# Performance work log

Measured on AMD Instinct MI355X. Metric: run time of the kernel, lower is better.

## Reference

```python
import jax, jax.numpy as jnp
import numpy as np

IMG = 224
BLK = 8
POOL = 7


def dct_matrix(n=BLK):
    # Orthonormal DCT-II matrix: dct(v, norm='ortho') == D @ v
    k = jnp.arange(n, dtype=jnp.float32)[:, None]
    m = jnp.arange(n, dtype=jnp.float32)[None, :]
    D = jnp.cos(jnp.pi * (2.0 * m + 1.0) * k / (2.0 * n)) * jnp.sqrt(2.0 / n)
    return D.at[0].mul(1.0 / jnp.sqrt(2.0))


def conv3x3(x, w, b):
    # NCHW, OIHW, stride 1, SAME padding
    y = jax.lax.conv_general_dilated(x, w, (1, 1), 'SAME',
                                     dimension_numbers=('NCHW', 'OIHW', 'NCHW'))
    return y + b[None, :, None, None]


def adaptive_pool7(x):
    # [B,C,224,224] -> [B,C,7,7] via mean over 32x32 windows
    B, C, H, W = x.shape
    return x.reshape(B, C, POOL, H // POOL, POOL, W // POOL).mean(axis=(3, 5))


def setup_inputs() -> dict:
    key = jax.random.key(0)
    ks = jax.random.split(key, 7)
    B = 32
    x = jax.random.uniform(ks[0], (B, 3, IMG, IMG), dtype=jnp.float32)
    s = 0.02
    return {
        'x': x,
        'dct_w': jax.random.normal(ks[1], (64, 3, 3, 3), jnp.float32) * s,
        'dct_b': jnp.zeros((64,), jnp.float32),
        'fft_w': jax.random.normal(ks[2], (64, 6, 3, 3), jnp.float32) * s,
        'fft_b': jnp.zeros((64,), jnp.float32),
        'fc_w': jax.random.normal(ks[3], (512, 2 * 64 * POOL * POOL), jnp.float32) * s,
        'fc_b': jnp.zeros((512,), jnp.float32),
    }


def reference(x, dct_w, dct_b, fft_w, fft_b, fc_w, fc_b):
    B = x.shape[0]
    # ---- DCT branch ----
    # grayscale (RGB2GRAY) scaled to 0..255 (uint8 cast omitted for differentiability)
    gray = (0.299 * x[:, 0] + 0.587 * x[:, 1] + 0.114 * x[:, 2]) * 255.0  # [B,H,W]
    nb = (IMG - BLK) // BLK  # 27: loop range(0, H-8, 8) skips the last block row/col
    g = gray[:, :nb * BLK, :nb * BLK].reshape(B, nb, BLK, nb, BLK)
    blocks = g.transpose(0, 1, 3, 2, 4).reshape(B, nb * nb, BLK, BLK)
    D = dct_matrix()
    dct_blocks = jnp.einsum('ij,bnjk,lk->bnil', D, blocks, D)  # 2D ortho DCT per block
    dct_img = dct_blocks.mean(axis=1)  # [B,8,8]
    dct_resized = jax.image.resize(dct_img, (B, IMG, IMG), method='linear')
    dct_in = jnp.broadcast_to(dct_resized[:, None], (B, 3, IMG, IMG))
    dct_pooled = adaptive_pool7(conv3x3(dct_in, dct_w, dct_b)).reshape(B, -1)

    # ---- FFT branch ----
    f = jnp.fft.fft2(x)  # [B,3,H,W] complex
    # channel order: real0, imag0, real1, imag1, real2, imag2
    fft_in = jnp.stack([f.real.astype(jnp.float32), f.imag.astype(jnp.float32)],
                       axis=2).reshape(B, 6, IMG, IMG)
    fft_pooled = adaptive_pool7(conv3x3(fft_in, fft_w, fft_b)).reshape(B, -1)

    combined = jnp.concatenate([dct_pooled, fft_pooled], axis=1)  # [B,6272]
    return jax.nn.relu(combined @ fc_w.T + fc_b)
```

## Files before the change

kernel.cpp:

```cpp
#include <hip/hip_runtime.h>
#include <math.h>

#define IMG 224
#define NR  21

__device__ __forceinline__ void range_lohi(int r, int& lo, int& hi) {
    int py = r / 3, s = (r % 3) - 1;
    lo = 32 * py + s; hi = lo + 32;
    if (lo < 0) lo = 0;
    if (hi > IMG) hi = IMG;
}

__device__ __forceinline__ float2 geom_range(int lo, int len, int y,
                                             const float* c0, const float* s0) {
    if (y == 0) return make_float2((float)len, 0.f);
    int i0 = (lo * y) % IMG;
    int iL = (len * y) % IMG;
    float w0x = c0[i0], w0y = s0[i0];
    float wLx = c0[iL], wLy = s0[iL];
    float w1x = c0[y],  w1y = s0[y];
    float nx = w0x * (1.f - wLx) + w0y * wLy;
    float ny = w0y * (1.f - wLx) - w0x * wLy;
    float dx = 1.f - w1x, dy = -w1y;
    float inv = 1.f / (dx * dx + dy * dy);
    return make_float2((nx * dx + ny * dy) * inv, (ny * dx - nx * dy) * inv);
}

__device__ __forceinline__ void build_cis(float* c0, float* s0, int t) {
    if (t < IMG) {
        double ang = 2.0 * M_PI * (double)t / (double)IMG;
        c0[t] = (float)cos(ang);
        s0[t] = (float)(-sin(ang));
    }
}

__global__ __launch_bounds__(256) void ka_rowdft_gray(const float* __restrict__ x,
        const float* __restrict__ dct_w,
        float2* __restrict__ T, float* __restrict__ meansum,
        float* __restrict__ afold_g, float* __restrict__ Dm_g,
        float* __restrict__ wsum3_g)
{
    __shared__ __align__(16) char smem[39424];
    int t = threadIdx.x;
    int blk = blockIdx.x;

    if (blk < 336) {
        float2* sA = (float2*)smem;
        float*  c0 = (float*)(smem + 37632);
        float*  s0 = c0 + IMG;
        build_cis(c0, s0, t);
        __syncthreads();
        for (int i = t; i < NR * IMG; i += 256) {
            int r = i / IMG, y = i % IMG;
            int lo, hi; range_lohi(r, lo, hi);
            sA[i] = geom_range(lo, hi - lo, y, c0, s0);
        }
        __syncthreads();

        int part = t >> 6;
        int lane = t & 63;
        int row = blk * 64 + lane;
        const float* src = x + (size_t)row * IMG + part * 56;

        float2 acc[NR];
        #pragma unroll
        for (int c = 0; c < NR; ++c) acc[c] = make_float2(0.f, 0.f);

        for (int i = 0; i < 56; i += 4) {
            float4 v = *(const float4*)(src + i);
            #pragma unroll
            for (int c = 0; c < NR; ++c) {
                const float2* ap = &sA[c * IMG + part * 56 + i];
                float2 a0 = ap[0], a1 = ap[1], a2 = ap[2], a3 = ap[3];
                acc[c].x += v.x * a0.x + v.y * a1.x + v.z * a2.x + v.w * a3.x;
                acc[c].y += v.x * a0.y + v.y * a1.y + v.z * a2.y + v.w * a3.y;
            }
        }

        __syncthreads();
        float2* red = (float2*)smem;
        if (part > 0) {
            float2* dst = red + ((size_t)(part - 1) * 64 + lane) * NR;
            #pragma unroll
            for (int c = 0; c < NR; ++c) dst[c] = acc[c];
        }
        __syncthreads();
        if (part == 0) {
            #pragma unroll
            for (int c = 0; c < NR; ++c) {
                float2 s = acc[c];
                float2 p1 = red[((size_t)0 * 64 + lane) * NR + c];
                float2 p2 = red[((size_t)1 * 64 + lane) * NR + c];
                float2 p3 = red[((size_t)2 * 64 + lane) * NR + c];
                s.x += p1.x + p2.x + p3.x;
                s.y += p1.y + p2.y + p3.y;
                T[(size_t)row * NR + c] = s;
            }
        }
    } else if (blk < 592) {
        int bb = blk - 336;
        int b = bb >> 3, j = bb & 7;
        float* sm = (float*)smem;
        if (t < 216) {
            const float* pr = x + (size_t)(b * 3 + 0) * IMG * IMG;
            const float* pg = x + (size_t)(b * 3 + 1) * IMG * IMG;
            const float* pb = x + (size_t)(b * 3 + 2) * IMG * IMG;
            float acc = 0.f;
            for (int by = 0; by < 27; ++by) {
                int o = (8 * by + j) * IMG + t;
                acc += 76.245f * pr[o] + 149.685f * pg[o] + 29.07f * pb[o];
            }
            sm[t] = acc;
        }
        __syncthreads();
        if (t < 8) {
            float s = 0.f;
            for (int q = t; q < 216; q += 8) s += sm[q];
            meansum[(b * 8 + j) * 8 + t] = s;
        }
    } else {
        if (t < NR * 8) {
            int r = t / 8, j = t % 8;
            int lo, hi; range_lohi(r, lo, hi);
            double s = 0.0;
            for (int y = lo; y < hi; ++y) {
                double sf = (y + 0.5) / 28.0 - 0.5;
                double w = 1.0 - fabs(sf - (double)j);
                if (w < 0.0) w = 0.0;
                double tot = 0.0;
                for (int jj = 0; jj < 8; ++jj) {
                    double wj = 1.0 - fabs(sf - (double)jj);
                    if (wj > 0.0) tot += wj;
                }
                s += w / tot;
            }
            afold_g[t] = (float)s;
        }
        if (t >= 192 && t < 256) {
            int i = t - 192, k = i / 8, m = i % 8;
            double v = cos(M_PI * (2.0 * m + 1.0) * k / 16.0) * 0.5;
            if (k == 0) v *= 0.70710678118654752440;
            Dm_g[i] = (float)v;
        }
        for (int i = t; i < 64 * 9; i += 256) {
            int cout = i / 9, q = i % 9;
            float s = 0.f;
            for (int cin = 0; cin < 3; ++cin) s += dct_w[(cout * 3 + cin) * 9 + q];
            wsum3_g[i] = s;
        }
    }
}

__global__ __launch_bounds__(256) void kb_fold(const float2* __restrict__ T,
        float2* __restrict__ rs2)
{
    __shared__ __align__(16) char smem[39424];
    float*  c0  = (float*)smem;
    float*  s0  = c0 + IMG;
    float2* sAh = (float2*)(smem + 1792);
    float2* sT  = (float2*)(smem + 20608);

    int blk = blockIdx.x, t = threadIdx.x;
    int b = blk / 6, rem = blk % 6;
    int cin = rem >> 1, half = rem & 1;

    build_cis(c0, s0, t);
    __syncthreads();
    for (int i = t; i < NR * 112; i += 256) {
        int rr = i / 112, y = half * 112 + (i % 112);
        int lo, hi; range_lohi(rr, lo, hi);
        sAh[i] = geom_range(lo, hi - lo, y, c0, s0);
    }
    const float2* Tbase = T + ((size_t)(b * 3 + cin) * IMG + half * 112) * NR;
    for (int i = t; i < 112 * NR; i += 256) sT[i] = Tbase[i];
    __syncthreads();

    float2* dst = rs2 + (size_t)((b * 3 + cin) * 2 + half) * NR * NR;
    for (int p = t; p < NR * NR; p += 256) {
        int rr = p / NR, cc = p % NR;
        float re = 0.f, im = 0.f;
        const float2* arow = &sAh[rr * 112];
        for (int y = 0; y < 112; ++y) {
            float2 a  = arow[y];
            float2 tv = sT[y * NR + cc];
            re += a.x * tv.x - a.y * tv.y;
            im += a.x * tv.y + a.y * tv.x;
        }
        dst[p] = make_float2(re, im);
    }
}

__global__ __launch_bounds__(256) void kb_asm(const float2* __restrict__ rs2,
        const float* __restrict__ meansum, const float* __restrict__ afold_g,
        const float* __restrict__ Dm_g, const float* __restrict__ wsum3_g,
        const float* __restrict__ dct_b, const float* __restrict__ fft_w,
        const float* __restrict__ fft_b, float* __restrict__ PT)
{
    __shared__ __align__(16) char smem[24576];
    int blk = blockIdx.x, t = threadIdx.x;
    int b = blk >> 1, which = blk & 1;
    const float inv = 1.0f / 1024.0f;

    if (which == 0) {
        float* WSd  = (float*)smem;
        float* Msc  = WSd + 441;
        float* dimg = Msc + 64;
        float* Ds   = dimg + 64;
        float* af   = Ds + 64;
        float* sws  = af + 168;
        if (t < 64) { Ds[t] = Dm_g[t]; Msc[t] = meansum[b * 64 + t] * (1.0f / 729.0f); }
        if (t < NR * 8) af[t] = afold_g[t];
        for (int i = t; i < 64 * 9; i += 256) sws[i] = wsum3_g[i];
        __syncthreads();
        if (t < 64) {
            int i = t / 8, l = t % 8;
            float s = 0.f;
            for (int j = 0; j < 8; ++j) {
                float rj = 0.f;
                for (int k = 0; k < 8; ++k) rj += Msc[j * 8 + k] * Ds[l * 8 + k];
                s += Ds[i * 8 + j] * rj;
            }
            dimg[t] = s;
        }
        __syncthreads();
        for (int p = t; p < NR * NR; p += 256) {
            int rr = p / NR, cc = p % NR;
            float s = 0.f;
            for (int j = 0; j < 8; ++j) {
                float rj = 0.f;
                for (int k = 0; k < 8; ++k) rj += dimg[j * 8 + k] * af[cc * 8 + k];
                s += af[rr * 8 + j] * rj;
            }
            WSd[p] = s;
        }
        __syncthreads();
        for (int i = t; i < 3136; i += 256) {
            int cout = i / 49, q = i % 49, py = q / 7, px = q % 7;
            float s = 0.f;
            #pragma unroll
            for (int ky = 0; ky < 3; ++ky)
                #pragma unroll
                for (int kx = 0; kx < 3; ++kx)
                    s += sws[cout * 9 + ky * 3 + kx] * WSd[(py * 3 + ky) * NR + (px * 3 + kx)];
            PT[(size_t)i * 32 + b] = dct_b[cout] + s * inv;
        }
    } else {
        float2* RSs = (float2*)smem;
        float*  sfw = (float*)(smem + 10584);
        for (int i = t; i < 3 * NR * NR; i += 256) {
            int cin = i / (NR * NR), p = i % (NR * NR);
            float2 v0 = rs2[(size_t)((b * 3 + cin) * 2 + 0) * NR * NR + p];
            float2 v1 = rs2[(size_t)((b * 3 + cin) * 2 + 1) * NR * NR + p];
            RSs[i] = make_float2(v0.x + v1.x, v0.y + v1.y);
        }
        for (int i = t; i < 64 * 6 * 9; i += 256) sfw[i] = fft_w[i];
        __syncthreads();
        for (int i = t; i < 3136; i += 256) {
            int cout = i / 49, q = i % 49, py = q / 7, px = q % 7;
            float s = 0.f;
            for (int cin = 0; cin < 3; ++cin) {
                #pragma unroll
                for (int ky = 0; ky < 3; ++ky)
                    #pragma unroll
                    for (int kx = 0; kx < 3; ++kx) {
                        float2 v = RSs[cin * NR * NR + (py * 3 + ky) * NR + (px * 3 + kx)];
                        const float* wp = &sfw[(cout * 6 + 2 * cin) * 9 + ky * 3 + kx];
                        s += wp[0] * v.x + wp[9] * v.y;
                    }
            }
            PT[(size_t)(3136 + i) * 32 + b] = fft_b[cout] + s * inv;
        }
    }
}

__global__ __launch_bounds__(256) void kc_fc(const float* __restrict__ PT,
        const float* __restrict__ fc_w, float* __restrict__ part)
{
    int oc = blockIdx.x / 14;
    int kc = blockIdx.x % 14;
    int t = threadIdx.x;
    int b = t & 31, sub = t >> 5;
    int o0 = oc * 4;
    int k0 = kc * 448 + sub * 56;

    const float* w0 = fc_w + (size_t)(o0 + 0) * 6272 + k0;
    const float* w1 = fc_w + (size_t)(o0 + 1) * 6272 + k0;
    const float* w2 = fc_w + (size_t)(o0 + 2) * 6272 + k0;
    const float* w3 = fc_w + (size_t)(o0 + 3) * 6272 + k0;
    const float* p  = PT + (size_t)k0 * 32 + b;

    float a0 = 0.f, a1 = 0.f, a2 = 0.f, a3 = 0.f;
    #pragma unroll 2
    for (int k = 0; k < 56; k += 4) {
        float4 v0 = *(const float4*)(w0 + k);
        float4 v1 = *(const float4*)(w1 + k);
        float4 v2 = *(const float4*)(w2 + k);
        float4 v3 = *(const float4*)(w3 + k);
        float p0 = p[(k + 0) * 32];
        float p1 = p[(k + 1) * 32];
        float p2 = p[(k + 2) * 32];
        float p3 = p[(k + 3) * 32];
        a0 += p0 * v0.x + p1 * v0.y + p2 * v0.z + p3 * v0.w;
        a1 += p0 * v1.x + p1 * v1.y + p2 * v1.z + p3 * v1.w;
        a2 += p0 * v2.x + p1 * v2.y + p2 * v2.z + p3 * v2.w;
        a3 += p0 * v3.x + p1 * v3.y + p2 * v3.z + p3 * v3.w;
    }

    __shared__ float sm[8 * 128];
    sm[sub * 128 +  0 + b] = a0;
    sm[sub * 128 + 32 + b] = a1;
    sm[sub * 128 + 64 + b] = a2;
    sm[sub * 128 + 96 + b] = a3;
    __syncthreads();
    if (t < 128) {
        int oi = t >> 5, b2 = t & 31;
        float s = 0.f;
        #pragma unroll
        for (int c = 0; c < 8; ++c) s += sm[c * 128 + oi * 32 + b2];
        part[(size_t)kc * 16384 + (size_t)(o0 + oi) * 32 + b2] = s;
    }
}

__global__ __launch_bounds__(256) void kc_out(const float* __restrict__ part,
        const float* __restrict__ fc_b, float* __restrict__ out)
{
    int idx = blockIdx.x * 256 + threadIdx.x;
    int o = idx >> 5, b = idx & 31;
    float s = fc_b[o];
    #pragma unroll
    for (int c = 0; c < 14; ++c) s += part[(size_t)c * 16384 + idx];
    out[(size_t)b * 512 + o] = fmaxf(s, 0.f);
}

extern "C" void kernel_launch(void* const* d_in, const int* in_sizes, int n_in,
                              void* d_out, int out_size, void* d_ws, size_t ws_size,
                              hipStream_t stream)
{
    const float* x     = (const float*)d_in[0];
    const float* dct_w = (const float*)d_in[1];
    const float* dct_b = (const float*)d_in[2];
    const float* fft_w = (const float*)d_in[3];
    const float* fft_b = (const float*)d_in[4];
    const float* fc_w  = (const float*)d_in[5];
    const float* fc_b  = (const float*)d_in[6];
    float* out = (float*)d_out;

    char* ws = (char*)d_ws;
    size_t off = 0;
    auto alloc = [&](size_t bytes) {
        char* p = ws + off;
        off = (off + bytes + 255) & ~(size_t)255;
        return p;
    };
    float2* T       = (float2*)alloc((size_t)21504 * NR * 8);
    float*  meansum = (float*) alloc(32 * 64 * 4);
    float*  afold_g = (float*) alloc(NR * 8 * 4);
    float*  Dm_g    = (float*) alloc(64 * 4);
    float*  wsum3_g = (float*) alloc(64 * 9 * 4);
    float2* rs2     = (float2*)alloc((size_t)192 * NR * NR * 8);
    float*  PT      = (float*) alloc((size_t)6272 * 32 * 4);
    float*  part    = (float*) alloc((size_t)14 * 512 * 32 * 4);
    (void)ws_size; (void)in_sizes; (void)n_in; (void)out_size;

    hipLaunchKernelGGL(ka_rowdft_gray, dim3(593),  dim3(256), 0, stream,
                       x, dct_w, T, meansum, afold_g, Dm_g, wsum3_g);
    hipLaunchKernelGGL(kb_fold,        dim3(192),  dim3(256), 0, stream, T, rs2);
    hipLaunchKernelGGL(kb_asm,         dim3(64),   dim3(256), 0, stream,
                       rs2, meansum, afold_g, Dm_g, wsum3_g, dct_b, fft_w, fft_b, PT);
    hipLaunchKernelGGL(kc_fc,          dim3(1792), dim3(256), 0, stream, PT, fc_w, part);
    hipLaunchKernelGGL(kc_out,         dim3(64),   dim3(256), 0, stream, part, fc_b, out);
}
```

Baseline: 147.0 us.

## Exploit real-input DFT symmetry and precompute twiddle-range table in separate kernel

Moves construction of the summed-twiddle coefficient table out of every row-DFT block into a tiny pre-kernel that writes real and imaginary tables to global memory. The row DFT now folds each real input row into symmetric (x[n]+x[N-n]) and antisymmetric parts, so only half the coefficients (113 of 224) are needed per output and the multiply count is roughly halved. This removes the per-block redundant table build and two barriers, and reads coefficients from global/cache instead of shared memory. It adds an extra kernel launch and relies on the range-summed coefficients having the conjugate symmetry that the split assumes.

```diff
diff --git a/kernel.cpp b/kernel.cpp
--- a/kernel.cpp
+++ b/kernel.cpp
@@ -34,50 +34,76 @@
     }
 }
 
+__global__ __launch_bounds__(256) void k0_tab(float* __restrict__ are,
+                                              float* __restrict__ aim)
+{
+    __shared__ float c0[IMG], s0[IMG];
+    int t = threadIdx.x;
+    build_cis(c0, s0, t);
+    __syncthreads();
+    int r = blockIdx.x;
+    int lo, hi; range_lohi(r, lo, hi);
+    if (t < 116) {
+        float2 a = (t < 113) ? geom_range(lo, hi - lo, t, c0, s0)
+                             : make_float2(0.f, 0.f);
+        are[r * 116 + t] = a.x;
+        aim[r * 116 + t] = a.y;
+    }
+}
+
 __global__ __launch_bounds__(256) void ka_rowdft_gray(const float* __restrict__ x,
         const float* __restrict__ dct_w,
+        const float* __restrict__ are, const float* __restrict__ aim,
         float2* __restrict__ T, float* __restrict__ meansum,
         float* __restrict__ afold_g, float* __restrict__ Dm_g,
         float* __restrict__ wsum3_g)
 {
-    __shared__ __align__(16) char smem[39424];
+    __shared__ __align__(16) char smem[32256];
     int t = threadIdx.x;
     int blk = blockIdx.x;
 
     if (blk < 336) {
-        float2* sA = (float2*)smem;
-        float*  c0 = (float*)(smem + 37632);
-        float*  s0 = c0 + IMG;
-        build_cis(c0, s0, t);
-        __syncthreads();
-        for (int i = t; i < NR * IMG; i += 256) {
-            int r = i / IMG, y = i % IMG;
-            int lo, hi; range_lohi(r, lo, hi);
-            sA[i] = geom_range(lo, hi - lo, y, c0, s0);
-        }
-        __syncthreads();
-
-        int part = t >> 6;
+        int part = __builtin_amdgcn_readfirstlane((t >> 6) & 3);
         int lane = t & 63;
         int row = blk * 64 + lane;
-        const float* src = x + (size_t)row * IMG + part * 56;
+        const float* src = x + (size_t)row * IMG;
+        int base0 = part * 28;
+
+        float sv[28], dv[28];
+        #pragma unroll
+        for (int ci = 0; ci < 7; ++ci) {
+            int base = base0 + 4 * ci;
+            float4 f = *(const float4*)(src + base);
+            float fj[4] = { f.x, f.y, f.z, f.w };
+            #pragma unroll
+            for (int j = 0; j < 4; ++j) {
+                int n = base + j;
+                float xm = (n == 0) ? 0.f : src[IMG - n];
+                sv[4 * ci + j] = fj[j] + xm;
+                dv[4 * ci + j] = fj[j] - xm;
+            }
+        }
+        float x112 = src[112];
 
         float2 acc[NR];
-        #pragma unroll
-        for (int c = 0; c < NR; ++c) acc[c] = make_float2(0.f, 0.f);
-
-        for (int i = 0; i < 56; i += 4) {
-            float4 v = *(const float4*)(src + i);
+        for (int c = 0; c < NR; ++c) {
+            const float* arp = are + c * 116 + base0;
+            const float* aip = aim + c * 116 + base0;
+            float re = 0.f, im = 0.f;
             #pragma unroll
-            for (int c = 0; c < NR; ++c) {
-                const float2* ap = &sA[c * IMG + part * 56 + i];
-                float2 a0 = ap[0], a1 = ap[1], a2 = ap[2], a3 = ap[3];
-                acc[c].x += v.x * a0.x + v.y * a1.x + v.z * a2.x + v.w * a3.x;
-                acc[c].y += v.x * a0.y + v.y * a1.y + v.z * a2.y + v.w * a3.y;
-            }
-        }
-
-        __syncthreads();
+            for (int ci = 0; ci < 7; ++ci) {
+                float4 a4 = *(const float4*)(arp + 4 * ci);
+                float4 b4 = *(const float4*)(aip + 4 * ci);
+                re += sv[4*ci+0]*a4.x + sv[4*ci+1]*a4.y + sv[4*ci+2]*a4.z + sv[4*ci+3]*a4.w;
+                im += dv[4*ci+0]*b4.x + dv[4*ci+1]*b4.y + dv[4*ci+2]*b4.z + dv[4*ci+3]*b4.w;
+            }
+            if (part == 0) {
+                re += x112 * arp[112];
+                im += x112 * aip[112];
+            }
+            acc[c] = make_float2(re, im);
+        }
+
         float2* red = (float2*)smem;
         if (part > 0) {
             float2* dst = red + ((size_t)(part - 1) * 64 + lane) * NR;
@@ -353,6 +379,8 @@
         return p;
     };
     float2* T       = (float2*)alloc((size_t)21504 * NR * 8);
+    float*  are     = (float*) alloc((size_t)NR * 116 * 4);
+    float*  aim     = (float*) alloc((size_t)NR * 116 * 4);
     float*  meansum = (float*) alloc(32 * 64 * 4);
     float*  afold_g = (float*) alloc(NR * 8 * 4);
     float*  Dm_g    = (float*) alloc(64 * 4);
@@ -362,8 +390,9 @@
     float*  part    = (float*) alloc((size_t)14 * 512 * 32 * 4);
     (void)ws_size; (void)in_sizes; (void)n_in; (void)out_size;
 
+    hipLaunchKernelGGL(k0_tab,         dim3(21),   dim3(256), 0, stream, are, aim);
     hipLaunchKernelGGL(ka_rowdft_gray, dim3(593),  dim3(256), 0, stream,
-                       x, dct_w, T, meansum, afold_g, Dm_g, wsum3_g);
+                       x, dct_w, are, aim, T, meansum, afold_g, Dm_g, wsum3_g);
     hipLaunchKernelGGL(kb_fold,        dim3(192),  dim3(256), 0, stream, T, rs2);
     hipLaunchKernelGGL(kb_asm,         dim3(64),   dim3(256), 0, stream,
                        rs2, meansum, afold_g, Dm_g, wsum3_g, dct_b, fft_w, fft_b, PT);
```

New measurement: 143.5 us. 2.4% less time.
